# Kernel tuning notes

Measured on AMD Instinct MI355X. Metric: run time of the kernel, lower is better.

## Reference

```python
import jax, jax.numpy as jnp
import numpy as np

N = 10000           # nodes
E = 320000          # edges
H = 128             # hidden_channels
L = 4               # num_layers
NUM_GRAPHS = 64
NUM_CLASSES = 10
MSG_EPS = 1e-7      # GENConv message epsilon


def layer_norm(x, g, b, eps=1e-5):
    mu = x.mean(-1, keepdims=True)
    var = x.var(-1, keepdims=True)
    return (x - mu) / jnp.sqrt(var + eps) * g + b


def setup_inputs() -> dict:
    key = jax.random.key(0)
    ks = jax.random.split(key, 10)
    def rn(k, shape, scale=0.05):
        return jax.random.normal(k, shape, jnp.float32) * scale
    return {
        "x": jax.random.normal(ks[0], (N, H), jnp.float32),
        "edge_attr": jax.random.normal(ks[1], (E, H), jnp.float32),
        "enc_W": rn(ks[2], (H, H)), "enc_b": jnp.zeros((H,), jnp.float32),
        "t": jnp.ones((L,), jnp.float32),                      # learnable softmax temperature per GENConv
        "W1": rn(ks[3], (L, H, 2 * H)), "b1": jnp.zeros((L, 2 * H), jnp.float32),
        "mlp_ln_g": jnp.ones((L, 2 * H), jnp.float32), "mlp_ln_b": jnp.zeros((L, 2 * H), jnp.float32),
        "W2": rn(ks[4], (L, 2 * H, H)), "b2": jnp.zeros((L, H), jnp.float32),
        "ln_g": jnp.ones((L, H), jnp.float32), "ln_b": jnp.zeros((L, H), jnp.float32),
        "lin_W": rn(ks[5], (H, NUM_CLASSES)), "lin_b": jnp.zeros((NUM_CLASSES,), jnp.float32),
        "edge_index": jax.random.randint(ks[6], (2, E), 0, N),
        "batch": jnp.sort(jax.random.randint(ks[7], (N,), 0, NUM_GRAPHS)),
    }


def genconv(x, src, dst, edge_attr, t, W1, b1, g1, be1, W2, b2):
    # GENConv, aggr='softmax': msg = relu(x_j + e) + eps; scatter-softmax over dst
    m = jax.nn.relu(x[src] + edge_attr) + MSG_EPS          # [E, H]
    logit = m * t
    mx = jax.ops.segment_max(logit, dst, num_segments=N)   # [N, H]
    ex = jnp.exp(logit - mx[dst])
    den = jax.ops.segment_sum(ex, dst, num_segments=N)
    alpha = ex / den[dst]                                   # per-edge softmax weight
    agg = jax.ops.segment_sum(m * alpha, dst, num_segments=N)  # [N, H]
    h = agg + x                                             # root skip inside GENConv
    # MLP: Lin(H,2H) -> LayerNorm -> ReLU -> Lin(2H,H)
    h = jax.nn.relu(layer_norm(h @ W1 + b1, g1, be1))
    return h @ W2 + b2


def reference(x, edge_attr, enc_W, enc_b, t, W1, b1, mlp_ln_g, mlp_ln_b, W2, b2, ln_g, ln_b, lin_W, lin_b, edge_index, batch):
    src, dst = edge_index[0], edge_index[1]
    h = x @ enc_W + enc_b
    # layers[0]: conv only
    h = genconv(h, src, dst, edge_attr, t[0], W1[0], b1[0], mlp_ln_g[0], mlp_ln_b[0], W2[0], b2[0])
    # layers[1:]: res+ block  x = x + conv(dropout(act(norm(x))))  (dropout=eval identity)
    for i in range(1, L):
        r = jax.nn.relu(layer_norm(h, ln_g[i], ln_b[i]))
        h = h + genconv(r, src, dst, edge_attr, t[i], W1[i], b1[i], mlp_ln_g[i], mlp_ln_b[i], W2[i], b2[i])
    h = jax.nn.relu(layer_norm(h, ln_g[0], ln_b[0]))       # layers[0].act(layers[0].norm(x))
    pooled = jax.ops.segment_sum(h, batch, num_segments=NUM_GRAPHS)  # global_add_pool
    return pooled @ lin_W + lin_b, pooled
```

## Files before the change

### kernel.cpp

```cpp
#include <hip/hip_runtime.h>
#include <hip/hip_bf16.h>

#define N_NODES 10000
#define N_EDGES 320000
#define H 128
#define H2 256
#define NLAYERS 4
#define NG 64
#define NC 10
#define MSG_EPS 1e-7f
#define LN_EPS 1e-5f

typedef __attribute__((ext_vector_type(8))) short bf16x8;
typedef __attribute__((ext_vector_type(4))) float f32x4;

__device__ __forceinline__ short f2bf(float f) {
    union { float f; unsigned u; } x; x.f = f;
    unsigned r = x.u + 0x7FFFu + ((x.u >> 16) & 1u);
    return (short)(r >> 16);
}
__device__ __forceinline__ unsigned short f2bfu(float f) {
    union { float f; unsigned u; } x; x.f = f;
    unsigned r = x.u + 0x7FFFu + ((x.u >> 16) & 1u);
    return (unsigned short)(r >> 16);
}
__device__ __forceinline__ float bf2f(unsigned short u) {
    union { unsigned u; float f; } x; x.u = ((unsigned)u) << 16;
    return x.f;
}


__global__ __launch_bounds__(256) void count_kernel(const int* __restrict__ dst,
                                                    int* __restrict__ counts) {
    int e = blockIdx.x * 256 + threadIdx.x;
    if (e < N_EDGES) atomicAdd(&counts[dst[e]], 1);
}

__global__ __launch_bounds__(256) void scan_kernel(const int* __restrict__ counts,
                                                   int* __restrict__ off,
                                                   int* __restrict__ cursor) {
    __shared__ int part[256];
    int tid = threadIdx.x;
    const int CH = (N_NODES + 255) / 256;
    int base = tid * CH;
    int s = 0;
    for (int i = 0; i < CH; ++i) {
        int idx = base + i;
        if (idx < N_NODES) s += counts[idx];
    }
    part[tid] = s;
    __syncthreads();
    for (int d = 1; d < 256; d <<= 1) {
        int t = (tid >= d) ? part[tid - d] : 0;
        __syncthreads();
        part[tid] += t;
        __syncthreads();
    }
    int run = part[tid] - s;
    for (int i = 0; i < CH; ++i) {
        int idx = base + i;
        if (idx < N_NODES) {
            off[idx] = run;
            cursor[idx] = run;
            run += counts[idx];
        }
    }
    if (tid == 255) off[N_NODES] = run;
}

__global__ __launch_bounds__(256) void scatter_kernel(const int* __restrict__ src,
                                                      const int* __restrict__ dst,
                                                      int* __restrict__ cursor,
                                                      int* __restrict__ perm_e,
                                                      int* __restrict__ perm_s) {
    int e = blockIdx.x * 256 + threadIdx.x;
    if (e < N_EDGES) {
        int p = atomicAdd(&cursor[dst[e]], 1);
        perm_e[p] = e;
        perm_s[p] = src[e];
    }
}


__global__ __launch_bounds__(256) void permute_ea_kernel(const float* __restrict__ ea,
                                                         const int* __restrict__ perm_e,
                                                         ushort* __restrict__ eap) {
    int g = threadIdx.x >> 5, lane = threadIdx.x & 31;
    int i = blockIdx.x * 8 + g;
    if (i < N_EDGES) {
        int e = perm_e[i];
        float4 v = ((const float4*)ea)[(size_t)e * 32 + lane];
        ushort4 o;
        o.x = f2bfu(v.x); o.y = f2bfu(v.y); o.z = f2bfu(v.z); o.w = f2bfu(v.w);
        ((ushort4*)eap)[(size_t)i * 32 + lane] = o;
    }
}


__global__ __launch_bounds__(256) void wconv_kernel(const float* __restrict__ W1,
                                                    const float* __restrict__ W2,
                                                    short* __restrict__ W1T,
                                                    short* __restrict__ W2T) {
    int idx = blockIdx.x * 256 + threadIdx.x;
    if (idx < NLAYERS * H * H2) {
        int k = idx & (H - 1);
        int c = (idx >> 7) & (H2 - 1);
        int l = idx >> 15;
        W1T[idx] = f2bf(W1[l * H * H2 + k * H2 + c]);
        int k2 = idx & (H2 - 1);
        int c2 = (idx >> 8) & (H - 1);
        W2T[idx] = f2bf(W2[l * H * H2 + k2 * H + c2]);
    }
}


__global__ __launch_bounds__(128) void encoder_kernel(const float* __restrict__ x,
                                                      const float* __restrict__ W,
                                                      const float* __restrict__ b,
                                                      float* __restrict__ h) {
    __shared__ float sx[8][H];
    int v0 = blockIdx.x * 8;
    int tid = threadIdx.x;
    for (int idx = tid; idx < 8 * H; idx += 128)
        sx[idx >> 7][idx & 127] = x[v0 * H + idx];
    __syncthreads();
    float y[8] = {0.f, 0.f, 0.f, 0.f, 0.f, 0.f, 0.f, 0.f};
    for (int k = 0; k < H; ++k) {
        float w = W[k * H + tid];
#pragma unroll
        for (int n = 0; n < 8; ++n) y[n] += sx[n][k] * w;
    }
    float bb = b[tid];
#pragma unroll
    for (int n = 0; n < 8; ++n) h[(v0 + n) * H + tid] = y[n] + bb;
}


__global__ __launch_bounds__(256) void ln_relu_kernel(const float* __restrict__ h,
                                                      const float* __restrict__ g,
                                                      const float* __restrict__ b,
                                                      float* __restrict__ out,
                                                      const int* __restrict__ batch,
                                                      float* __restrict__ pooled,
                                                      int do_pool) {
    int wave = threadIdx.x >> 6, lane = threadIdx.x & 63;
    int v = blockIdx.x * 4 + wave;
    if (v >= N_NODES) return;
    float2 x = ((const float2*)(h + (size_t)v * H))[lane];
    float s = x.x + x.y, sq = x.x * x.x + x.y * x.y;
    for (int d = 32; d; d >>= 1) {
        s += __shfl_down(s, d);
        sq += __shfl_down(sq, d);
    }
    s = __shfl(s, 0);
    sq = __shfl(sq, 0);
    float mu = s * (1.f / H);
    float var = sq * (1.f / H) - mu * mu;
    float rstd = rsqrtf(var + LN_EPS);
    float2 gg = ((const float2*)g)[lane];
    float2 bb = ((const float2*)b)[lane];
    float f0 = fmaxf((x.x - mu) * rstd * gg.x + bb.x, 0.f);
    float f1 = fmaxf((x.y - mu) * rstd * gg.y + bb.y, 0.f);
    if (do_pool) {
        float* p = pooled + (size_t)batch[v] * H + lane * 2;
        atomicAdd(p, f0);
        atomicAdd(p + 1, f1);
    } else {
        ((float2*)(out + (size_t)v * H))[lane] = make_float2(f0, f1);
    }
}


#define PROC(cc)                                           \
    {                                                      \
        float m = fmaxf(xv.cc + ev.cc, 0.f) + MSG_EPS;     \
        float exx = __expf(m * tl);                        \
        den.cc += exx;                                     \
        num.cc += m * exx;                                 \
    }

__device__ __forceinline__ float4 bf4(ushort4 u) {
    return make_float4(bf2f(u.x), bf2f(u.y), bf2f(u.z), bf2f(u.w));
}

__global__ __launch_bounds__(256) void edge_agg_kernel(const float* __restrict__ xcur,
                                                       const ushort* __restrict__ eap,
                                                       const int* __restrict__ off,
                                                       const int* __restrict__ perm_s,
                                                       const float* __restrict__ t, int l,
                                                       float* __restrict__ u) {
    int v = blockIdx.x;
    int tid = threadIdx.x;
    int g = tid >> 5;
    int lane = tid & 31;
    float tl = t[l];
    int b = off[v], e_end = off[v + 1];
    const float4* x4 = (const float4*)xcur;
    const ushort4* e4 = (const ushort4*)eap;
    float4 den = {0.f, 0.f, 0.f, 0.f}, num = {0.f, 0.f, 0.f, 0.f};

    int i = b + g;
    for (; i + 24 < e_end; i += 32) {
        int s0 = perm_s[i], s1 = perm_s[i + 8], s2 = perm_s[i + 16], s3 = perm_s[i + 24];
        float4 xv0 = x4[(size_t)s0 * 32 + lane];
        ushort4 eb0 = e4[(size_t)i * 32 + lane];
        float4 xv1 = x4[(size_t)s1 * 32 + lane];
        ushort4 eb1 = e4[(size_t)(i + 8) * 32 + lane];
        float4 xv2 = x4[(size_t)s2 * 32 + lane];
        ushort4 eb2 = e4[(size_t)(i + 16) * 32 + lane];
        float4 xv3 = x4[(size_t)s3 * 32 + lane];
        ushort4 eb3 = e4[(size_t)(i + 24) * 32 + lane];
        { float4 xv = xv0, ev = bf4(eb0); PROC(x) PROC(y) PROC(z) PROC(w) }
        { float4 xv = xv1, ev = bf4(eb1); PROC(x) PROC(y) PROC(z) PROC(w) }
        { float4 xv = xv2, ev = bf4(eb2); PROC(x) PROC(y) PROC(z) PROC(w) }
        { float4 xv = xv3, ev = bf4(eb3); PROC(x) PROC(y) PROC(z) PROC(w) }
    }
    for (; i < e_end; i += 8) {
        int s0 = perm_s[i];
        float4 xv = x4[(size_t)s0 * 32 + lane];
        float4 ev = bf4(e4[(size_t)i * 32 + lane]);
        PROC(x) PROC(y) PROC(z) PROC(w)
    }

    __shared__ float4 sden[8][32];
    __shared__ float4 snum[8][32];
    sden[g][lane] = den;
    snum[g][lane] = num;
    __syncthreads();
#pragma unroll
    for (int step = 4; step >= 1; step >>= 1) {
        if (g < step) {
            float4 a = sden[g][lane], b2 = sden[g + step][lane];
            a.x += b2.x; a.y += b2.y; a.z += b2.z; a.w += b2.w;
            sden[g][lane] = a;
            float4 c = snum[g][lane], d2 = snum[g + step][lane];
            c.x += d2.x; c.y += d2.y; c.z += d2.z; c.w += d2.w;
            snum[g][lane] = c;
        }
        __syncthreads();
    }
    if (g == 0) {
        float4 dn = sden[0][lane], nm = snum[0][lane];
        float4 xv = x4[(size_t)v * 32 + lane];
        float4 o;
        o.x = (dn.x > 0.f ? nm.x / dn.x : 0.f) + xv.x;
        o.y = (dn.y > 0.f ? nm.y / dn.y : 0.f) + xv.y;
        o.z = (dn.z > 0.f ? nm.z / dn.z : 0.f) + xv.z;
        o.w = (dn.w > 0.f ? nm.w / dn.w : 0.f) + xv.w;
        ((float4*)u)[(size_t)v * 32 + lane] = o;
    }
}


__global__ __launch_bounds__(256) void mlp_mfma_kernel(const float* __restrict__ u,
                                                       const float* __restrict__ hin,
                                                       float* __restrict__ hout,
                                                       const short* __restrict__ W1T,
                                                       const float* __restrict__ b1,
                                                       const float* __restrict__ g1,
                                                       const float* __restrict__ be1,
                                                       const short* __restrict__ W2T,
                                                       const float* __restrict__ b2,
                                                       int residual) {
    __shared__ short Ub[32 * 128];
    __shared__ short Ab[32 * 256];
    __shared__ float redv[2][32][4];
    __shared__ float musig[2][32];
    int tid = threadIdx.x;
    int wave = tid >> 6, lane = tid & 63;
    int l15 = lane & 15, lg = lane >> 4;
    int v0 = blockIdx.x * 32;
    int nrow = N_NODES - v0; if (nrow > 32) nrow = 32;

    for (int c = tid; c < 32 * 16; c += 256) {
        int row = c >> 4, ch = c & 15;
        bf16x8 val = {0, 0, 0, 0, 0, 0, 0, 0};
        if (row < nrow) {
            const float4* up = (const float4*)(u + (size_t)(v0 + row) * H + ch * 8);
            float4 f0 = up[0], f1 = up[1];
            val[0] = f2bf(f0.x); val[1] = f2bf(f0.y); val[2] = f2bf(f0.z); val[3] = f2bf(f0.w);
            val[4] = f2bf(f1.x); val[5] = f2bf(f1.y); val[6] = f2bf(f1.z); val[7] = f2bf(f1.w);
        }
        *(bf16x8*)&Ub[row * 128 + ((ch ^ (row & 7)) * 8)] = val;
    }
    __syncthreads();

    int nc0 = wave * 64;
    f32x4 acc[2][4];
#pragma unroll
    for (int mi = 0; mi < 2; ++mi)
#pragma unroll
        for (int ni = 0; ni < 4; ++ni) acc[mi][ni] = (f32x4){0.f, 0.f, 0.f, 0.f};
#pragma unroll
    for (int ks = 0; ks < 4; ++ks) {
        bf16x8 af[2], bfr[4];
#pragma unroll
        for (int mi = 0; mi < 2; ++mi) {
            int row = mi * 16 + l15;
            int ch = ks * 4 + lg;
            af[mi] = *(const bf16x8*)&Ub[row * 128 + ((ch ^ (row & 7)) * 8)];
        }
#pragma unroll
        for (int ni = 0; ni < 4; ++ni) {
            int col = nc0 + ni * 16 + l15;
            bfr[ni] = *(const bf16x8*)&W1T[col * H + ks * 32 + lg * 8];
        }
#pragma unroll
        for (int mi = 0; mi < 2; ++mi)
#pragma unroll
            for (int ni = 0; ni < 4; ++ni)
                acc[mi][ni] = __builtin_amdgcn_mfma_f32_16x16x32_bf16(af[mi], bfr[ni], acc[mi][ni], 0, 0, 0);
    }

    float bcol[4];
#pragma unroll
    for (int ni = 0; ni < 4; ++ni) bcol[ni] = b1[nc0 + ni * 16 + l15];
#pragma unroll
    for (int mi = 0; mi < 2; ++mi) {
#pragma unroll
        for (int j = 0; j < 4; ++j) {
            float s = 0.f, q = 0.f;
#pragma unroll
            for (int ni = 0; ni < 4; ++ni) {
                float y = acc[mi][ni][j] + bcol[ni];
                acc[mi][ni][j] = y;
                s += y;
                q += y * y;
            }
#pragma unroll
            for (int m = 8; m >= 1; m >>= 1) {
                s += __shfl_xor(s, m);
                q += __shfl_xor(q, m);
            }
            if (l15 == 0) {
                int row = mi * 16 + lg * 4 + j;
                redv[0][row][wave] = s;
                redv[1][row][wave] = q;
            }
        }
    }
    __syncthreads();
    if (tid < 32) {
        float S = redv[0][tid][0] + redv[0][tid][1] + redv[0][tid][2] + redv[0][tid][3];
        float Q = redv[1][tid][0] + redv[1][tid][1] + redv[1][tid][2] + redv[1][tid][3];
        float mu = S * (1.f / H2);
        float var = Q * (1.f / H2) - mu * mu;
        musig[0][tid] = mu;
        musig[1][tid] = rsqrtf(var + LN_EPS);
    }
    __syncthreads();

    float gcol[4], becol[4];
#pragma unroll
    for (int ni = 0; ni < 4; ++ni) {
        gcol[ni] = g1[nc0 + ni * 16 + l15];
        becol[ni] = be1[nc0 + ni * 16 + l15];
    }
#pragma unroll
    for (int mi = 0; mi < 2; ++mi)
#pragma unroll
        for (int j = 0; j < 4; ++j) {
            int row = mi * 16 + lg * 4 + j;
            float mu = musig[0][row], rs = musig[1][row];
#pragma unroll
            for (int ni = 0; ni < 4; ++ni) {
                int col = nc0 + ni * 16 + l15;
                float a = fmaxf((acc[mi][ni][j] - mu) * rs * gcol[ni] + becol[ni], 0.f);
                int ch = col >> 3, o8 = col & 7;
                Ab[row * 256 + ((ch ^ (row & 7)) * 8) + o8] = f2bf(a);
            }
        }
    __syncthreads();

    int nc2 = wave * 32;
    f32x4 acc2[2][2];
#pragma unroll
    for (int mi = 0; mi < 2; ++mi)
#pragma unroll
        for (int ni = 0; ni < 2; ++ni) acc2[mi][ni] = (f32x4){0.f, 0.f, 0.f, 0.f};
#pragma unroll
    for (int ks = 0; ks < 8; ++ks) {
        bf16x8 af[2], bfr[2];
#pragma unroll
        for (int mi = 0; mi < 2; ++mi) {
            int row = mi * 16 + l15;
            int ch = ks * 4 + lg;
            af[mi] = *(const bf16x8*)&Ab[row * 256 + ((ch ^ (row & 7)) * 8)];
        }
#pragma unroll
        for (int ni = 0; ni < 2; ++ni) {
            int col = nc2 + ni * 16 + l15;
            bfr[ni] = *(const bf16x8*)&W2T[col * H2 + ks * 32 + lg * 8];
        }
#pragma unroll
        for (int mi = 0; mi < 2; ++mi)
#pragma unroll
            for (int ni = 0; ni < 2; ++ni)
                acc2[mi][ni] = __builtin_amdgcn_mfma_f32_16x16x32_bf16(af[mi], bfr[ni], acc2[mi][ni], 0, 0, 0);
    }

#pragma unroll
    for (int ni = 0; ni < 2; ++ni) {
        int col = nc2 + ni * 16 + l15;
        float bb = b2[col];
#pragma unroll
        for (int mi = 0; mi < 2; ++mi)
#pragma unroll
            for (int j = 0; j < 4; ++j) {
                int row = mi * 16 + lg * 4 + j;
                if (row < nrow) {
                    size_t gi = (size_t)(v0 + row) * H + col;
                    float z = acc2[mi][ni][j] + bb;
                    hout[gi] = residual ? hin[gi] + z : z;
                }
            }
    }
}


__global__ __launch_bounds__(640) void logits_kernel(const float* __restrict__ pooled,
                                                     const float* __restrict__ W,
                                                     const float* __restrict__ b,
                                                     float* __restrict__ out) {
    int tid = threadIdx.x;
    if (tid < NG * NC) {
        int g = tid / NC, c = tid % NC;
        float acc = b[c];
        for (int k = 0; k < H; ++k) acc += pooled[g * H + k] * W[k * NC + c];
        out[g * NC + c] = acc;
    }
    for (int idx = tid; idx < NG * H; idx += 640) out[NG * NC + idx] = pooled[idx];
}


extern "C" void kernel_launch(void* const* d_in, const int* in_sizes, int n_in,
                              void* d_out, int out_size, void* d_ws, size_t ws_size,
                              hipStream_t stream) {
    const float* x     = (const float*)d_in[0];
    const float* ea    = (const float*)d_in[1];
    const float* enc_W = (const float*)d_in[2];
    const float* enc_b = (const float*)d_in[3];
    const float* t     = (const float*)d_in[4];
    const float* W1    = (const float*)d_in[5];
    const float* b1    = (const float*)d_in[6];
    const float* g1    = (const float*)d_in[7];
    const float* be1   = (const float*)d_in[8];
    const float* W2    = (const float*)d_in[9];
    const float* b2    = (const float*)d_in[10];
    const float* lng   = (const float*)d_in[11];
    const float* lnb   = (const float*)d_in[12];
    const float* linW  = (const float*)d_in[13];
    const float* linb  = (const float*)d_in[14];
    const int*   ei    = (const int*)d_in[15];
    const int*   batch = (const int*)d_in[16];
    const int* src = ei;
    const int* dst = ei + N_EDGES;
    float* out = (float*)d_out;

    short* W1T   = (short*)d_ws;
    short* W2T   = W1T + NLAYERS * H * H2;
    ushort* eap  = (ushort*)(W2T + NLAYERS * H * H2);
    float* h     = (float*)(eap + (size_t)N_EDGES * H);
    float* r      = h + (size_t)N_NODES * H;
    float* u      = r + (size_t)N_NODES * H;
    float* pooled = u + (size_t)N_NODES * H;
    int* counts = (int*)(pooled + NG * H);
    int* off    = counts + N_NODES;
    int* cursor = off + N_NODES + 16;
    int* perm_e = cursor + N_NODES;
    int* perm_s = perm_e + N_EDGES;

    hipMemsetAsync(counts, 0, N_NODES * sizeof(int), stream);
    hipMemsetAsync(pooled, 0, NG * H * sizeof(float), stream);

    count_kernel<<<(N_EDGES + 255) / 256, 256, 0, stream>>>(dst, counts);
    scan_kernel<<<1, 256, 0, stream>>>(counts, off, cursor);
    scatter_kernel<<<(N_EDGES + 255) / 256, 256, 0, stream>>>(src, dst, cursor, perm_e, perm_s);
    permute_ea_kernel<<<N_EDGES / 8, 256, 0, stream>>>(ea, perm_e, eap);
    wconv_kernel<<<(NLAYERS * H * H2 + 255) / 256, 256, 0, stream>>>(W1, W2, W1T, W2T);

    encoder_kernel<<<N_NODES / 8, 128, 0, stream>>>(x, enc_W, enc_b, h);

    for (int l = 0; l < NLAYERS; ++l) {
        const float* xcur;
        if (l == 0) {
            xcur = h;
        } else {
            ln_relu_kernel<<<(N_NODES + 3) / 4, 256, 0, stream>>>(h, lng + l * H, lnb + l * H, r,
                                                                  nullptr, nullptr, 0);
            xcur = r;
        }
        edge_agg_kernel<<<N_NODES, 256, 0, stream>>>(xcur, eap, off, perm_s, t, l, u);
        mlp_mfma_kernel<<<(N_NODES + 31) / 32, 256, 0, stream>>>(
            u, h, h, W1T + (size_t)l * H * H2, b1 + l * H2, g1 + l * H2, be1 + l * H2,
            W2T + (size_t)l * H * H2, b2 + l * H, l > 0);
    }

    ln_relu_kernel<<<(N_NODES + 3) / 4, 256, 0, stream>>>(h, lng, lnb, nullptr, batch, pooled, 1);
    logits_kernel<<<1, 640, 0, stream>>>(pooled, linW, linb, out);
}
```

Baseline: 612.5 us.

## Fuse LayerNorm/ReLU/pool into MLP epilogue, bf16 node features, one-wave-per-node aggregation

```diff
diff --git a/kernel.cpp b/kernel.cpp
--- a/kernel.cpp
+++ b/kernel.cpp
@@ -71,28 +71,28 @@
 __global__ __launch_bounds__(256) void scatter_kernel(const int* __restrict__ src,
                                                       const int* __restrict__ dst,
                                                       int* __restrict__ cursor,
-                                                      int* __restrict__ perm_e,
-                                                      int* __restrict__ perm_s) {
+                                                      int* __restrict__ perm_s,
+                                                      int* __restrict__ invp) {
     int e = blockIdx.x * 256 + threadIdx.x;
     if (e < N_EDGES) {
         int p = atomicAdd(&cursor[dst[e]], 1);
-        perm_e[p] = e;
         perm_s[p] = src[e];
+        invp[e] = p;
     }
 }
 
 
 __global__ __launch_bounds__(256) void permute_ea_kernel(const float* __restrict__ ea,
-                                                         const int* __restrict__ perm_e,
-                                                         ushort* __restrict__ eap) {
+                                                         const int* __restrict__ invp,
+                                                         ushort* __restrict__ eapb) {
     int g = threadIdx.x >> 5, lane = threadIdx.x & 31;
-    int i = blockIdx.x * 8 + g;
-    if (i < N_EDGES) {
-        int e = perm_e[i];
+    int e = blockIdx.x * 8 + g;
+    if (e < N_EDGES) {
+        int p = invp[e];
         float4 v = ((const float4*)ea)[(size_t)e * 32 + lane];
         ushort4 o;
         o.x = f2bfu(v.x); o.y = f2bfu(v.y); o.z = f2bfu(v.z); o.w = f2bfu(v.w);
-        ((ushort4*)eap)[(size_t)i * 32 + lane] = o;
+        ((ushort4*)eapb)[(size_t)p * 32 + lane] = o;
     }
 }
 
@@ -117,7 +117,8 @@
 __global__ __launch_bounds__(128) void encoder_kernel(const float* __restrict__ x,
                                                       const float* __restrict__ W,
                                                       const float* __restrict__ b,
-                                                      float* __restrict__ h) {
+                                                      float* __restrict__ h,
+                                                      ushort* __restrict__ hb) {
     __shared__ float sx[8][H];
     int v0 = blockIdx.x * 8;
     int tid = threadIdx.x;
@@ -132,127 +133,75 @@
     }
     float bb = b[tid];
 #pragma unroll
-    for (int n = 0; n < 8; ++n) h[(v0 + n) * H + tid] = y[n] + bb;
-}
-
-
-__global__ __launch_bounds__(256) void ln_relu_kernel(const float* __restrict__ h,
-                                                      const float* __restrict__ g,
-                                                      const float* __restrict__ b,
-                                                      float* __restrict__ out,
-                                                      const int* __restrict__ batch,
-                                                      float* __restrict__ pooled,
-                                                      int do_pool) {
-    int wave = threadIdx.x >> 6, lane = threadIdx.x & 63;
-    int v = blockIdx.x * 4 + wave;
-    if (v >= N_NODES) return;
-    float2 x = ((const float2*)(h + (size_t)v * H))[lane];
-    float s = x.x + x.y, sq = x.x * x.x + x.y * x.y;
-    for (int d = 32; d; d >>= 1) {
-        s += __shfl_down(s, d);
-        sq += __shfl_down(sq, d);
-    }
-    s = __shfl(s, 0);
-    sq = __shfl(sq, 0);
-    float mu = s * (1.f / H);
-    float var = sq * (1.f / H) - mu * mu;
-    float rstd = rsqrtf(var + LN_EPS);
-    float2 gg = ((const float2*)g)[lane];
-    float2 bb = ((const float2*)b)[lane];
-    float f0 = fmaxf((x.x - mu) * rstd * gg.x + bb.x, 0.f);
-    float f1 = fmaxf((x.y - mu) * rstd * gg.y + bb.y, 0.f);
-    if (do_pool) {
-        float* p = pooled + (size_t)batch[v] * H + lane * 2;
-        atomicAdd(p, f0);
-        atomicAdd(p + 1, f1);
-    } else {
-        ((float2*)(out + (size_t)v * H))[lane] = make_float2(f0, f1);
-    }
-}
-
-
-#define PROC(cc)                                           \
-    {                                                      \
-        float m = fmaxf(xv.cc + ev.cc, 0.f) + MSG_EPS;     \
-        float exx = __expf(m * tl);                        \
-        den.cc += exx;                                     \
-        num.cc += m * exx;                                 \
-    }
-
-__device__ __forceinline__ float4 bf4(ushort4 u) {
-    return make_float4(bf2f(u.x), bf2f(u.y), bf2f(u.z), bf2f(u.w));
-}
-
-__global__ __launch_bounds__(256) void edge_agg_kernel(const float* __restrict__ xcur,
-                                                       const ushort* __restrict__ eap,
+    for (int n = 0; n < 8; ++n) {
+        float z = y[n] + bb;
+        h[(v0 + n) * H + tid] = z;
+        hb[(v0 + n) * H + tid] = f2bfu(z);
+    }
+}
+
+
+#define PROCB(xu, eu, cc)                                        \
+    {                                                            \
+        float m = fmaxf(bf2f(xu.cc) + bf2f(eu.cc), 0.f) + MSG_EPS; \
+        float exx = __expf(m * tl);                              \
+        den.cc += exx;                                           \
+        num.cc += m * exx;                                       \
+    }
+#define PROC4B(xu, eu) PROCB(xu, eu, x) PROCB(xu, eu, y) PROCB(xu, eu, z) PROCB(xu, eu, w)
+
+__global__ __launch_bounds__(256) void edge_agg_kernel(const ushort* __restrict__ xb,
+                                                       const ushort* __restrict__ eapb,
                                                        const int* __restrict__ off,
                                                        const int* __restrict__ perm_s,
                                                        const float* __restrict__ t, int l,
-                                                       float* __restrict__ u) {
-    int v = blockIdx.x;
+                                                       ushort* __restrict__ ub) {
     int tid = threadIdx.x;
-    int g = tid >> 5;
-    int lane = tid & 31;
+    int v = blockIdx.x * 4 + (tid >> 6);
+    int lane = tid & 63, half = lane >> 5, l32 = lane & 31;
     float tl = t[l];
     int b = off[v], e_end = off[v + 1];
-    const float4* x4 = (const float4*)xcur;
-    const ushort4* e4 = (const ushort4*)eap;
+    const ushort4* x4 = (const ushort4*)xb;
+    const ushort4* e4 = (const ushort4*)eapb;
     float4 den = {0.f, 0.f, 0.f, 0.f}, num = {0.f, 0.f, 0.f, 0.f};
 
-    int i = b + g;
-    for (; i + 24 < e_end; i += 32) {
-        int s0 = perm_s[i], s1 = perm_s[i + 8], s2 = perm_s[i + 16], s3 = perm_s[i + 24];
-        float4 xv0 = x4[(size_t)s0 * 32 + lane];
-        ushort4 eb0 = e4[(size_t)i * 32 + lane];
-        float4 xv1 = x4[(size_t)s1 * 32 + lane];
-        ushort4 eb1 = e4[(size_t)(i + 8) * 32 + lane];
-        float4 xv2 = x4[(size_t)s2 * 32 + lane];
-        ushort4 eb2 = e4[(size_t)(i + 16) * 32 + lane];
-        float4 xv3 = x4[(size_t)s3 * 32 + lane];
-        ushort4 eb3 = e4[(size_t)(i + 24) * 32 + lane];
-        { float4 xv = xv0, ev = bf4(eb0); PROC(x) PROC(y) PROC(z) PROC(w) }
-        { float4 xv = xv1, ev = bf4(eb1); PROC(x) PROC(y) PROC(z) PROC(w) }
-        { float4 xv = xv2, ev = bf4(eb2); PROC(x) PROC(y) PROC(z) PROC(w) }
-        { float4 xv = xv3, ev = bf4(eb3); PROC(x) PROC(y) PROC(z) PROC(w) }
-    }
-    for (; i < e_end; i += 8) {
+    int i = b + half;
+    for (; i + 6 < e_end; i += 8) {
+        int s0 = perm_s[i], s1 = perm_s[i + 2], s2 = perm_s[i + 4], s3 = perm_s[i + 6];
+        ushort4 xv0 = x4[(size_t)s0 * 32 + l32], ev0 = e4[(size_t)i * 32 + l32];
+        ushort4 xv1 = x4[(size_t)s1 * 32 + l32], ev1 = e4[(size_t)(i + 2) * 32 + l32];
+        ushort4 xv2 = x4[(size_t)s2 * 32 + l32], ev2 = e4[(size_t)(i + 4) * 32 + l32];
+        ushort4 xv3 = x4[(size_t)s3 * 32 + l32], ev3 = e4[(size_t)(i + 6) * 32 + l32];
+        PROC4B(xv0, ev0)
+        PROC4B(xv1, ev1)
+        PROC4B(xv2, ev2)
+        PROC4B(xv3, ev3)
+    }
+    for (; i < e_end; i += 2) {
         int s0 = perm_s[i];
-        float4 xv = x4[(size_t)s0 * 32 + lane];
-        float4 ev = bf4(e4[(size_t)i * 32 + lane]);
-        PROC(x) PROC(y) PROC(z) PROC(w)
-    }
-
-    __shared__ float4 sden[8][32];
-    __shared__ float4 snum[8][32];
-    sden[g][lane] = den;
-    snum[g][lane] = num;
-    __syncthreads();
-#pragma unroll
-    for (int step = 4; step >= 1; step >>= 1) {
-        if (g < step) {
-            float4 a = sden[g][lane], b2 = sden[g + step][lane];
-            a.x += b2.x; a.y += b2.y; a.z += b2.z; a.w += b2.w;
-            sden[g][lane] = a;
-            float4 c = snum[g][lane], d2 = snum[g + step][lane];
-            c.x += d2.x; c.y += d2.y; c.z += d2.z; c.w += d2.w;
-            snum[g][lane] = c;
-        }
-        __syncthreads();
-    }
-    if (g == 0) {
-        float4 dn = sden[0][lane], nm = snum[0][lane];
-        float4 xv = x4[(size_t)v * 32 + lane];
-        float4 o;
-        o.x = (dn.x > 0.f ? nm.x / dn.x : 0.f) + xv.x;
-        o.y = (dn.y > 0.f ? nm.y / dn.y : 0.f) + xv.y;
-        o.z = (dn.z > 0.f ? nm.z / dn.z : 0.f) + xv.z;
-        o.w = (dn.w > 0.f ? nm.w / dn.w : 0.f) + xv.w;
-        ((float4*)u)[(size_t)v * 32 + lane] = o;
-    }
-}
-
-
-__global__ __launch_bounds__(256) void mlp_mfma_kernel(const float* __restrict__ u,
+        ushort4 xv = x4[(size_t)s0 * 32 + l32];
+        ushort4 ev = e4[(size_t)i * 32 + l32];
+        PROC4B(xv, ev)
+    }
+
+    den.x += __shfl_xor(den.x, 32); den.y += __shfl_xor(den.y, 32);
+    den.z += __shfl_xor(den.z, 32); den.w += __shfl_xor(den.w, 32);
+    num.x += __shfl_xor(num.x, 32); num.y += __shfl_xor(num.y, 32);
+    num.z += __shfl_xor(num.z, 32); num.w += __shfl_xor(num.w, 32);
+
+    if (half == 0) {
+        ushort4 xvb = x4[(size_t)v * 32 + l32];
+        ushort4 ob;
+        ob.x = f2bfu((den.x > 0.f ? num.x / den.x : 0.f) + bf2f(xvb.x));
+        ob.y = f2bfu((den.y > 0.f ? num.y / den.y : 0.f) + bf2f(xvb.y));
+        ob.z = f2bfu((den.z > 0.f ? num.z / den.z : 0.f) + bf2f(xvb.z));
+        ob.w = f2bfu((den.w > 0.f ? num.w / den.w : 0.f) + bf2f(xvb.w));
+        ((ushort4*)ub)[(size_t)v * 32 + l32] = ob;
+    }
+}
+
+
+__global__ __launch_bounds__(256) void mlp_mfma_kernel(const ushort* __restrict__ ub,
                                                        const float* __restrict__ hin,
                                                        float* __restrict__ hout,
                                                        const short* __restrict__ W1T,
@@ -261,7 +210,13 @@
                                                        const float* __restrict__ be1,
                                                        const short* __restrict__ W2T,
                                                        const float* __restrict__ b2,
-                                                       int residual) {
+                                                       int residual,
+                                                       const float* __restrict__ gn,
+                                                       const float* __restrict__ bn,
+                                                       ushort* __restrict__ rbout,
+                                                       int final_pool,
+                                                       const int* __restrict__ batch,
+                                                       float* __restrict__ pooled) {
     __shared__ short Ub[32 * 128];
     __shared__ short Ab[32 * 256];
     __shared__ float redv[2][32][4];
@@ -275,12 +230,8 @@
     for (int c = tid; c < 32 * 16; c += 256) {
         int row = c >> 4, ch = c & 15;
         bf16x8 val = {0, 0, 0, 0, 0, 0, 0, 0};
-        if (row < nrow) {
-            const float4* up = (const float4*)(u + (size_t)(v0 + row) * H + ch * 8);
-            float4 f0 = up[0], f1 = up[1];
-            val[0] = f2bf(f0.x); val[1] = f2bf(f0.y); val[2] = f2bf(f0.z); val[3] = f2bf(f0.w);
-            val[4] = f2bf(f1.x); val[5] = f2bf(f1.y); val[6] = f2bf(f1.z); val[7] = f2bf(f1.w);
-        }
+        if (row < nrow)
+            val = *(const bf16x8*)&ub[(size_t)(v0 + row) * H + ch * 8];
         *(bf16x8*)&Ub[row * 128 + ((ch ^ (row & 7)) * 8)] = val;
     }
     __syncthreads();
@@ -399,6 +350,7 @@
                 acc2[mi][ni] = __builtin_amdgcn_mfma_f32_16x16x32_bf16(af[mi], bfr[ni], acc2[mi][ni], 0, 0, 0);
     }
 
+    float zz[2][2][4];
 #pragma unroll
     for (int ni = 0; ni < 2; ++ni) {
         int col = nc2 + ni * 16 + l15;
@@ -408,10 +360,55 @@
 #pragma unroll
             for (int j = 0; j < 4; ++j) {
                 int row = mi * 16 + lg * 4 + j;
+                size_t gi = (size_t)(v0 + row) * H + col;
+                float hv = (residual && row < nrow) ? hin[gi] : 0.f;
+                float z = acc2[mi][ni][j] + bb + hv;
+                zz[mi][ni][j] = z;
+                if (row < nrow) hout[gi] = z;
+            }
+    }
+#pragma unroll
+    for (int mi = 0; mi < 2; ++mi)
+#pragma unroll
+        for (int j = 0; j < 4; ++j) {
+            float s = zz[mi][0][j] + zz[mi][1][j];
+            float q = zz[mi][0][j] * zz[mi][0][j] + zz[mi][1][j] * zz[mi][1][j];
+#pragma unroll
+            for (int m = 8; m >= 1; m >>= 1) {
+                s += __shfl_xor(s, m);
+                q += __shfl_xor(q, m);
+            }
+            if (l15 == 0) {
+                int row = mi * 16 + lg * 4 + j;
+                redv[0][row][wave] = s;
+                redv[1][row][wave] = q;
+            }
+        }
+    __syncthreads();
+    if (tid < 32) {
+        float S = redv[0][tid][0] + redv[0][tid][1] + redv[0][tid][2] + redv[0][tid][3];
+        float Q = redv[1][tid][0] + redv[1][tid][1] + redv[1][tid][2] + redv[1][tid][3];
+        float mu = S * (1.f / H);
+        float var = Q * (1.f / H) - mu * mu;
+        musig[0][tid] = mu;
+        musig[1][tid] = rsqrtf(var + LN_EPS);
+    }
+    __syncthreads();
+#pragma unroll
+    for (int ni = 0; ni < 2; ++ni) {
+        int col = nc2 + ni * 16 + l15;
+        float gv = gn[col], bv = bn[col];
+#pragma unroll
+        for (int mi = 0; mi < 2; ++mi)
+#pragma unroll
+            for (int j = 0; j < 4; ++j) {
+                int row = mi * 16 + lg * 4 + j;
                 if (row < nrow) {
-                    size_t gi = (size_t)(v0 + row) * H + col;
-                    float z = acc2[mi][ni][j] + bb;
-                    hout[gi] = residual ? hin[gi] + z : z;
+                    float rn = fmaxf((zz[mi][ni][j] - musig[0][row]) * musig[1][row] * gv + bv, 0.f);
+                    if (final_pool)
+                        atomicAdd(&pooled[(size_t)batch[v0 + row] * H + col], rn);
+                    else
+                        rbout[(size_t)(v0 + row) * H + col] = f2bfu(rn);
                 }
             }
     }
@@ -457,45 +454,40 @@
     const int* dst = ei + N_EDGES;
     float* out = (float*)d_out;
 
-    short* W1T   = (short*)d_ws;
-    short* W2T   = W1T + NLAYERS * H * H2;
-    ushort* eap  = (ushort*)(W2T + NLAYERS * H * H2);
-    float* h     = (float*)(eap + (size_t)N_EDGES * H);
-    float* r      = h + (size_t)N_NODES * H;
-    float* u      = r + (size_t)N_NODES * H;
-    float* pooled = u + (size_t)N_NODES * H;
+    short*  W1T  = (short*)d_ws;
+    short*  W2T  = W1T + NLAYERS * H * H2;
+    ushort* eapb = (ushort*)(W2T + NLAYERS * H * H2);
+    ushort* xb   = eapb + (size_t)N_EDGES * H;
+    ushort* ub   = xb + (size_t)N_NODES * H;
+    float*  h    = (float*)(ub + (size_t)N_NODES * H);
+    float*  pooled = h + (size_t)N_NODES * H;
     int* counts = (int*)(pooled + NG * H);
     int* off    = counts + N_NODES;
     int* cursor = off + N_NODES + 16;
-    int* perm_e = cursor + N_NODES;
-    int* perm_s = perm_e + N_EDGES;
+    int* perm_s = cursor + N_NODES;
+    int* invp   = perm_s + N_EDGES;
 
     hipMemsetAsync(counts, 0, N_NODES * sizeof(int), stream);
     hipMemsetAsync(pooled, 0, NG * H * sizeof(float), stream);
 
     count_kernel<<<(N_EDGES + 255) / 256, 256, 0, stream>>>(dst, counts);
     scan_kernel<<<1, 256, 0, stream>>>(counts, off, cursor);
-    scatter_kernel<<<(N_EDGES + 255) / 256, 256, 0, stream>>>(src, dst, cursor, perm_e, perm_s);
-    permute_ea_kernel<<<N_EDGES / 8, 256, 0, stream>>>(ea, perm_e, eap);
+    scatter_kernel<<<(N_EDGES + 255) / 256, 256, 0, stream>>>(src, dst, cursor, perm_s, invp);
+    permute_ea_kernel<<<N_EDGES / 8, 256, 0, stream>>>(ea, invp, eapb);
     wconv_kernel<<<(NLAYERS * H * H2 + 255) / 256, 256, 0, stream>>>(W1, W2, W1T, W2T);
 
-    encoder_kernel<<<N_NODES / 8, 128, 0, stream>>>(x, enc_W, enc_b, h);
+    encoder_kernel<<<N_NODES / 8, 128, 0, stream>>>(x, enc_W, enc_b, h, xb);
 
     for (int l = 0; l < NLAYERS; ++l) {
-        const float* xcur;
-        if (l == 0) {
-            xcur = h;
-        } else {
-            ln_relu_kernel<<<(N_NODES + 3) / 4, 256, 0, stream>>>(h, lng + l * H, lnb + l * H, r,
-                                                                  nullptr, nullptr, 0);
-            xcur = r;
-        }
-        edge_agg_kernel<<<N_NODES, 256, 0, stream>>>(xcur, eap, off, perm_s, t, l, u);
+        edge_agg_kernel<<<N_NODES / 4, 256, 0, stream>>>(xb, eapb, off, perm_s, t, l, ub);
+        int final_pool = (l == NLAYERS - 1);
+        const float* gn = final_pool ? lng : lng + (l + 1) * H;
+        const float* bn = final_pool ? lnb : lnb + (l + 1) * H;
         mlp_mfma_kernel<<<(N_NODES + 31) / 32, 256, 0, stream>>>(
-            u, h, h, W1T + (size_t)l * H * H2, b1 + l * H2, g1 + l * H2, be1 + l * H2,
-            W2T + (size_t)l * H * H2, b2 + l * H, l > 0);
-    }
-
-    ln_relu_kernel<<<(N_NODES + 3) / 4, 256, 0, stream>>>(h, lng, lnb, nullptr, batch, pooled, 1);
+            ub, h, h, W1T + (size_t)l * H * H2, b1 + l * H2, g1 + l * H2, be1 + l * H2,
+            W2T + (size_t)l * H * H2, b2 + l * H, l > 0,
+            gn, bn, xb, final_pool, batch, pooled);
+    }
+
     logits_kernel<<<1, 640, 0, stream>>>(pooled, linW, linb, out);
 }
```

Result: faster. 571.1 us (-6.8%).
